# Performance work log

Hardware: AMD Instinct MI355X
Metric: run time of the kernel (lower is better)

Reference implementation:

```python
import jax, jax.numpy as jnp
import numpy as np

B = 512; S = 6; Q = 2            # meta-batch, n_way*k_shot, n_way*q_query
DIM = 64; IMG = 28; N_WAY = 2
HEADS = 4; HD = DIM // HEADS     # retrieval heads / head dim
EPS = 1e-5


def _pool_mat(inp, out):
    # exact torch AdaptiveAvgPool2d windowing as a matrix [out, inp]
    P = np.zeros((out, inp), np.float32)
    for i in range(out):
        s = (i * inp) // out
        e = -((-(i + 1) * inp) // out)
        P[i, s:e] = 1.0 / (e - s)
    return jnp.asarray(P)

P28 = _pool_mat(IMG, 8)  # 28 -> 8; subsequent 8 -> 8 pools are identity


def _gelu(x):
    return jax.nn.gelu(x, approximate=False)


def _conv(x, w, b):
    y = jax.lax.conv_general_dilated(x, w, (1, 1), ((1, 1), (1, 1)),
                                     dimension_numbers=('NCHW', 'OIHW', 'NCHW'))
    return y + b[None, :, None, None]


def _bn(x, p):
    # p rows: gamma, beta, running_mean, running_var (eval-mode BatchNorm2d)
    g, bt, m, v = p[0], p[1], p[2], p[3]
    sc = g / jnp.sqrt(v + EPS)
    return (x - m[None, :, None, None]) * sc[None, :, None, None] + bt[None, :, None, None]


def _img_in(x, c1w, c1b, bn1, c2w, c2b, bn2, c3w, c3b, bn3, c4w, c4b, bn4, lin_w):
    h = _bn(_conv(x, c1w, c1b), bn1)
    h = jnp.einsum('oi,ncij,pj->ncop', P28, h, P28)   # adaptive avg pool 28x28 -> 8x8
    h = _gelu(h)                                       # dropout is identity in eval
    h = _gelu(_bn(_conv(h, c2w, c2b), bn2))
    h = _gelu(_bn(_conv(h, c3w, c3b), bn3))
    h = _gelu(_bn(_conv(h, c4w, c4b), bn4))            # -> [N,1,8,8]
    h = h.reshape(h.shape[0], -1)                      # [N,64]
    return h @ lin_w.T                                 # Linear(64 -> DIM, no bias)


def _net(x, w1, w2):
    # x: [B,K,D]; w1,w2: [B,D,D] batched fast weights
    h = jnp.einsum('bed,bkd->bke', w1, x)
    ah = _gelu(h)
    y = jnp.einsum('bed,bkd->bke', w2, ah)
    return y, h


def _get_lor(x, w1, w2, r_q, r_k, r_v, r_o, ln_w, ln_b):
    b, k, _ = x.shape
    q, _ = _net(x, w1, w2)
    qh = jnp.einsum('nhd,bkd->bknh', r_q, q)
    sc = jnp.einsum('bknh,rnh->bknr', qh, r_k) / (HD ** 0.5)
    p = jax.nn.softmax(sc, axis=-1)
    lor = jnp.einsum('bknr,rnh->bknh', p, r_v).reshape(b, k, DIM)
    lor = jnp.einsum('de,bkd->bke', r_o, lor)
    z = lor + x
    mu = z.mean(-1, keepdims=True)
    var = ((z - mu) ** 2).mean(-1, keepdims=True)
    return (z - mu) / jnp.sqrt(var + EPS) * ln_w + ln_b


def _forward(query_w, sxs, qxs, inner_lr, c1w, c1b, bn1, c2w, c2b, bn2, c3w, c3b, bn3,
             c4w, c4b, bn4, lin_w, emb, w1, w2, tags, r_q, r_k, r_v, r_o, ln_w, ln_b,
             sys, qys):
    b = query_w.shape[0]
    s = sxs.shape[1]
    q = qxs.shape[1]
    feats = lambda im: _img_in(im.reshape(-1, 1, IMG, IMG), c1w, c1b, bn1, c2w, c2b,
                               bn2, c3w, c3b, bn3, c4w, c4b, bn4, lin_w)
    sx = feats(sxs).reshape(b, s, DIM)
    qx = feats(qxs).reshape(b, q, DIM)
    qe = tags[4]
    w1b = jnp.broadcast_to(w1, (b, DIM, DIM))
    w2b = jnp.broadcast_to(w2, (b, DIM, DIM))
    bound = sx + emb[sys]                                          # [B,S,D]
    # all 4 tag variants for all S shots in one vectorized get_lor call
    inp = (bound[:, :, None, :] + tags[:4][None, None]).reshape(b, s * 4, DIM)
    lors = _get_lor(inp, w1b, w2b, r_q, r_k, r_v, r_o, ln_w, ln_b).reshape(b, s, 4, DIM)
    l1s, r1s, l2s, r2s = lors[:, :, 0], lors[:, :, 1], lors[:, :, 2], lors[:, :, 3]
    qw1 = w1[None] + jnp.einsum('bsl,bsr->blr', l1s, r1s)
    qw2 = w2[None] + jnp.einsum('bsl,bsr->blr', l2s, r2s)
    preds, _ = _net(qx + qe, qw1, qw2)                             # [B,Q,D]
    logits = jnp.einsum('ld,bqd->bql', emb, preds).reshape(-1, N_WAY)
    labels = qys.reshape(-1)
    ls = jax.nn.log_softmax(logits)
    task_loss = -jnp.take_along_axis(ls, labels[:, None], axis=1).mean()
    n_correct = (jnp.argmax(logits, axis=1) == labels).sum()
    return task_loss, n_correct, b * q


def setup_inputs() -> dict:
    key = jax.random.key(0)
    ks = jax.random.split(key, 24)
    rn = lambda i, sh, sc=1.0: sc * jax.random.normal(ks[i], sh, jnp.float32)
    def bnp(i, c):
        k0, k1, k2 = jax.random.split(ks[i], 3)
        return jnp.stack([1.0 + 0.1 * jax.random.normal(k0, (c,)),
                          0.1 * jax.random.normal(k1, (c,)),
                          0.1 * jax.random.normal(k2, (c,)),
                          0.5 + jax.random.uniform(jax.random.fold_in(ks[i], 3), (c,))])
    return {
        'query_w': rn(0, (B, DIM)),
        'sxs': rn(1, (B, S, IMG * IMG)),
        'qxs': rn(2, (B, Q, IMG * IMG)),
        'inner_lr': jnp.float32(0.1),
        'c1w': rn(3, (32, 1, 3, 3), 0.3), 'c1b': rn(4, (32,), 0.1), 'bn1': bnp(5, 32),
        'c2w': rn(6, (32, 32, 3, 3), 0.06), 'c2b': rn(7, (32,), 0.1), 'bn2': bnp(8, 32),
        'c3w': rn(9, (32, 32, 3, 3), 0.06), 'c3b': rn(10, (32,), 0.1), 'bn3': bnp(11, 32),
        'c4w': rn(12, (1, 32, 3, 3), 0.06), 'c4b': rn(13, (1,), 0.1), 'bn4': bnp(14, 1),
        'lin_w': rn(15, (DIM, 64), 0.125),
        'emb': rn(16, (N_WAY, DIM), 0.125),
        'w1': rn(17, (DIM, DIM), 0.125),
        'w2': rn(18, (DIM, DIM), 0.125),
        'tags': rn(19, (8, DIM), 0.125),
        'r_q': rn(20, (HEADS, HD, DIM), 0.125),
        'r_k': rn(21, (16, HEADS, HD), 0.25),
        'r_v': rn(22, (16, HEADS, HD), 0.25),
        'r_o': rn(23, (DIM, DIM), 0.125),
        'ln_w': 0.001 * jnp.ones((DIM,), jnp.float32),
        'ln_b': jnp.zeros((DIM,), jnp.float32),
        'sys': jax.random.randint(jax.random.fold_in(key, 100), (B, S), 0, N_WAY),
        'qys': jax.random.randint(jax.random.fold_in(key, 101), (B, Q), 0, N_WAY),
    }


def reference(query_w, sxs, qxs, inner_lr, c1w, c1b, bn1, c2w, c2b, bn2, c3w, c3b, bn3,
              c4w, c4b, bn4, lin_w, emb, w1, w2, tags, r_q, r_k, r_v, r_o, ln_w, ln_b,
              sys, qys):
    task_loss, n_correct, n_q = _forward(query_w, sxs, qxs, inner_lr, c1w, c1b, bn1,
                                         c2w, c2b, bn2, c3w, c3b, bn3, c4w, c4b, bn4,
                                         lin_w, emb, w1, w2, tags, r_q, r_k, r_v, r_o,
                                         ln_w, ln_b, sys, qys)
    return (task_loss, task_loss, jnp.float32(0.0), n_correct, n_q)
```

## Files before the change

### kernel.cpp

```cpp
#include <hip/hip_runtime.h>
#include <math.h>

constexpr int NSUP = 3072;
constexpr float EPSF = 1e-5f;

constexpr int WS_W1B  = 0;
constexpr int WS_B1   = 1024;
constexpr int WS_W2B  = 1056;
constexpr int WS_W3B  = 5664;
constexpr int WS_W4B  = 10272;
constexpr int WS_B4   = 10416;
constexpr int WS_B2   = 10420;
constexpr int WS_B3   = 10452;
constexpr int WS_HW1  = 10484;
constexpr int WS_HW2  = 12788;
constexpr int WS_HRQ  = 15092;
constexpr int WS_HROT = 17396;
constexpr int WS_PART = 19700;
constexpr int WS_FEATS= 20724;

using short8 = __attribute__((ext_vector_type(8))) short;
using f32x4  = __attribute__((ext_vector_type(4))) float;

__device__ __forceinline__ float gelu_f(float x) {
    float z  = fabsf(x) * 0.70710678118654752440f;
    float t  = __builtin_amdgcn_rcpf(__builtin_fmaf(0.3275911f, z, 1.0f));
    float p  = t * __builtin_fmaf(t,
                 __builtin_fmaf(t,
                   __builtin_fmaf(t,
                     __builtin_fmaf(t, 1.061405429f, -1.453152027f),
                     1.421413741f),
                   -0.284496736f),
                 0.254829592f);
    float e  = __expf(-z * z);
    float er = __builtin_fmaf(-p, e, 1.0f);
    float s  = copysignf(er, x);
    return 0.5f * x * (1.0f + s);
}
__device__ __forceinline__ unsigned short f2bf(float f) {
    unsigned u = __float_as_uint(f);
    return (unsigned short)((u + 0x7FFFu + ((u >> 16) & 1u)) >> 16);
}
__device__ __forceinline__ float bflo(unsigned u) { return __uint_as_float(u << 16); }
__device__ __forceinline__ float bfhi(unsigned u) { return __uint_as_float(u & 0xffff0000u); }

__global__ void __launch_bounds__(256) precompute_kernel(
    const float* __restrict__ c1w, const float* __restrict__ c1b, const float* __restrict__ bn1,
    const float* __restrict__ c2w, const float* __restrict__ c2b, const float* __restrict__ bn2,
    const float* __restrict__ c3w, const float* __restrict__ c3b, const float* __restrict__ bn3,
    const float* __restrict__ c4w, const float* __restrict__ c4b, const float* __restrict__ bn4,
    const float* __restrict__ w1, const float* __restrict__ w2,
    const float* __restrict__ rq, const float* __restrict__ ro,
    float* __restrict__ ws)
{
    const int gid = blockIdx.x * 256 + threadIdx.x;
    const int gsz = gridDim.x * 256;

    unsigned short* w1b = (unsigned short*)(ws + WS_W1B);
    for (int v = gid; v < 2048; v += gsz) {
        int kt = v >> 10, rem = v & 1023, oc = rem >> 5, kk = rem & 31;
        int tap = kt * 32 + kk;
        unsigned short o = 0;
        if (tap < 36) {
            int tt = tap / 6, s = tap - tt * 6;
            float sum = 0.f;
            for (int di = 0; di < 3; ++di) {
                int a = tt - di; if (a < 0 || a > 3) continue;
                for (int dj = 0; dj < 3; ++dj) {
                    int bb = s - dj; if (bb < 0 || bb > 3) continue;
                    sum += c1w[oc * 9 + di * 3 + dj];
                }
            }
            float sc1 = bn1[oc] * rsqrtf(bn1[96 + oc] + EPSF);
            o = f2bf(sum * sc1 * (1.0f / 16.0f));
        }
        w1b[v] = o;
    }
    for (int c = gid; c < 32; c += gsz) {
        float sc1 = bn1[c] * rsqrtf(bn1[96 + c] + EPSF);
        ws[WS_B1 + c] = (c1b[c] - bn1[64 + c]) * sc1 + bn1[32 + c];
        float sc2 = bn2[c] * rsqrtf(bn2[96 + c] + EPSF);
        ws[WS_B2 + c] = (c2b[c] - bn2[64 + c]) * sc2 + bn2[32 + c];
        float sc3 = bn3[c] * rsqrtf(bn3[96 + c] + EPSF);
        ws[WS_B3 + c] = (c3b[c] - bn3[64 + c]) * sc3 + bn3[32 + c];
    }
    unsigned short* w2b = (unsigned short*)(ws + WS_W2B);
    unsigned short* w3b = (unsigned short*)(ws + WS_W3B);
    for (int v = gid; v < 9216; v += gsz) {
        int tap = v >> 10, oc = (v >> 5) & 31, ic = v & 31;
        float sc2 = bn2[oc] * rsqrtf(bn2[96 + oc] + EPSF);
        float sc3 = bn3[oc] * rsqrtf(bn3[96 + oc] + EPSF);
        w2b[v] = f2bf(c2w[oc * 288 + ic * 9 + tap] * sc2);
        w3b[v] = f2bf(c3w[oc * 288 + ic * 9 + tap] * sc3);
    }
    {
        unsigned short* w4b = (unsigned short*)(ws + WS_W4B);
        float sc4 = bn4[0] * rsqrtf(bn4[3] + EPSF);
        for (int v = gid; v < 288; v += gsz) {
            int tap = v >> 5, ic = v & 31;
            w4b[v] = f2bf(c4w[ic * 9 + tap] * sc4);
        }
        if (gid == 0) ws[WS_B4] = (c4b[0] - bn4[2]) * sc4 + bn4[1];
    }
    unsigned short* hw1 = (unsigned short*)(ws + WS_HW1);
    unsigned short* hw2 = (unsigned short*)(ws + WS_HW2);
    unsigned short* hrq = (unsigned short*)(ws + WS_HRQ);
    unsigned short* hro = (unsigned short*)(ws + WS_HROT);
    for (int v = gid; v < 4608; v += gsz) {
        int e = v / 72, d = v - e * 72;
        unsigned short a = 0, b = 0, c = 0, r = 0;
        if (d < 64) {
            a = f2bf(w1[e * 64 + d]);
            b = f2bf(w2[e * 64 + d]);
            c = f2bf(rq[e * 64 + d]);
            r = f2bf(ro[d * 64 + e]);
        }
        hw1[v] = a; hw2[v] = b; hrq[v] = c; hro[v] = r;
    }
}

__device__ __forceinline__ void conv32(unsigned short* __restrict__ A,
                                       const unsigned short* __restrict__ W,
                                       float bi0, float bi1, int col, int quad)
{
    f32x4 acc[4][2];
    #pragma unroll
    for (int mt = 0; mt < 4; ++mt) { acc[mt][0] = (f32x4){0,0,0,0}; acc[mt][1] = (f32x4){0,0,0,0}; }
    const unsigned short* abase[4];
    #pragma unroll
    for (int mt = 0; mt < 4; ++mt) {
        int px = mt * 16 + col;
        abase[mt] = A + ((px >> 3) * 10 + (px & 7)) * 32 + quad * 8;
    }
    #pragma unroll
    for (int dr = 0; dr < 3; ++dr)
        #pragma unroll
        for (int dc = 0; dc < 3; ++dc) {
            int tap = dr * 3 + dc;
            short8 b0 = *(const short8*)(W + (tap * 32 + col) * 32 + quad * 8);
            short8 b1 = *(const short8*)(W + (tap * 32 + 16 + col) * 32 + quad * 8);
            #pragma unroll
            for (int mt = 0; mt < 4; ++mt) {
                short8 a = *(const short8*)(abase[mt] + (dr * 10 + dc) * 32);
                acc[mt][0] = __builtin_amdgcn_mfma_f32_16x16x32_bf16(a, b0, acc[mt][0], 0, 0, 0);
                acc[mt][1] = __builtin_amdgcn_mfma_f32_16x16x32_bf16(a, b1, acc[mt][1], 0, 0, 0);
            }
        }
    #pragma unroll
    for (int mt = 0; mt < 4; ++mt)
        #pragma unroll
        for (int reg = 0; reg < 4; ++reg) {
            int px = mt * 16 + quad * 4 + reg;
            unsigned short* dst = A + (((px >> 3) + 1) * 10 + (px & 7) + 1) * 32;
            dst[col]      = f2bf(gelu_f(acc[mt][0][reg] + bi0));
            dst[col + 16] = f2bf(gelu_f(acc[mt][1][reg] + bi1));
        }
}

__global__ void __launch_bounds__(512, 4) feats_kernel(
    const float* __restrict__ sxs, const float* __restrict__ qxs,
    const float* __restrict__ lin_w, const float* __restrict__ ws,
    float* __restrict__ feats)
{
    __shared__ __align__(16) unsigned short sAct[8][3200];
    __shared__ __align__(16) unsigned short sWB[9216];
    __shared__ __align__(16) unsigned short sW4[288];
    __shared__ __align__(16) float sh4[8][64];

    const int t    = threadIdx.x;
    const int wv   = t >> 6;
    const int lane = t & 63;
    const int col  = lane & 15;
    const int quad = lane >> 4;
    const int n    = blockIdx.x * 8 + wv;

    unsigned short* A = sAct[wv];

    const uint4* w2v = (const uint4*)(ws + WS_W2B);
    uint4 pw0 = w2v[t];
    uint4 pw1 = w2v[t + 512];
    uint4 pw2 = {0, 0, 0, 0};
    if (t < 128) pw2 = w2v[t + 1024];

    {
        const float* img = (n < NSUP) ? (sxs + (size_t)n * 784) : (qxs + (size_t)(n - NSUP) * 784);
        const float4* sv = (const float4*)img;
        #pragma unroll
        for (int j = 0; j < 4; ++j) {
            int idx = j * 64 + lane;
            if (idx < 196) {
                float4 v = sv[idx];
                ushort4 o = { f2bf(v.x), f2bf(v.y), f2bf(v.z), f2bf(v.w) };
                *(ushort4*)(A + idx * 4) = o;
            }
        }
    }
    if (t < 256) ((uint4*)sWB)[t] = ((const uint4*)(ws + WS_W1B))[t];
    __syncthreads();

    {
        int ttj[8], ssj[8];
        #pragma unroll
        for (int j = 0; j < 8; ++j) {
            int k = quad * 8 + j;
            ttj[j] = k / 6; ssj[j] = k - ttj[j] * 6;
        }
        f32x4 acc[4][2];
        #pragma unroll
        for (int mt = 0; mt < 4; ++mt) { acc[mt][0] = (f32x4){0,0,0,0}; acc[mt][1] = (f32x4){0,0,0,0}; }

        short8 b00 = *(const short8*)(sWB + (0 * 32 + 0 * 16 + col) * 32 + quad * 8);
        short8 b01 = *(const short8*)(sWB + (0 * 32 + 1 * 16 + col) * 32 + quad * 8);
        short8 b10 = *(const short8*)(sWB + (1 * 32 + 0 * 16 + col) * 32 + quad * 8);
        short8 b11 = *(const short8*)(sWB + (1 * 32 + 1 * 16 + col) * 32 + quad * 8);

        #pragma unroll
        for (int mt = 0; mt < 4; ++mt) {
            int px = mt * 16 + col;
            int sr = (((px >> 3) * 7) >> 1) - 1;
            int sc = (((px & 7) * 7) >> 1) - 1;
            short8 a0;
            #pragma unroll
            for (int j = 0; j < 8; ++j) {
                int rr = sr + ttj[j], cc = sc + ssj[j];
                bool ok = ((unsigned)rr < 28u) && ((unsigned)cc < 28u);
                int off = ok ? (rr * 28 + cc) : 0;
                unsigned short hv = A[off];
                a0[j] = ok ? (short)hv : (short)0;
            }
            acc[mt][0] = __builtin_amdgcn_mfma_f32_16x16x32_bf16(a0, b00, acc[mt][0], 0, 0, 0);
            acc[mt][1] = __builtin_amdgcn_mfma_f32_16x16x32_bf16(a0, b01, acc[mt][1], 0, 0, 0);
            short8 a1 = {0,0,0,0,0,0,0,0};
            if (quad == 0) {
                #pragma unroll
                for (int j = 0; j < 4; ++j) {
                    int rr = sr + 5, cc = sc + 2 + j;
                    bool ok = ((unsigned)rr < 28u) && ((unsigned)cc < 28u);
                    int off = ok ? (rr * 28 + cc) : 0;
                    unsigned short hv = A[off];
                    a1[j] = ok ? (short)hv : (short)0;
                }
            }
            acc[mt][0] = __builtin_amdgcn_mfma_f32_16x16x32_bf16(a1, b10, acc[mt][0], 0, 0, 0);
            acc[mt][1] = __builtin_amdgcn_mfma_f32_16x16x32_bf16(a1, b11, acc[mt][1], 0, 0, 0);
        }

        {
            uint4 z4 = {0, 0, 0, 0};
            #pragma unroll
            for (int it = 0; it < 3; ++it) {
                int h = lane + it * 64;
                if (h < 144) {
                    int u4;
                    if (h < 40)      u4 = h;
                    else if (h < 80) u4 = 360 + (h - 40);
                    else {
                        int k = h - 80; int r = 1 + (k >> 3); int cj = k & 7;
                        u4 = r * 40 + ((cj >= 4) ? (32 + cj) : cj);
                    }
                    ((uint4*)A)[u4] = z4;
                }
            }
        }
        float bi0 = ws[WS_B1 + col], bi1 = ws[WS_B1 + 16 + col];
        #pragma unroll
        for (int mt = 0; mt < 4; ++mt)
            #pragma unroll
            for (int reg = 0; reg < 4; ++reg) {
                int px = mt * 16 + quad * 4 + reg;
                unsigned short* dst = A + (((px >> 3) + 1) * 10 + (px & 7) + 1) * 32;
                dst[col]      = f2bf(gelu_f(acc[mt][0][reg] + bi0));
                dst[col + 16] = f2bf(gelu_f(acc[mt][1][reg] + bi1));
            }
    }
    __syncthreads();

    {
        ((uint4*)sWB)[t]       = pw0;
        ((uint4*)sWB)[t + 512] = pw1;
        if (t < 128) ((uint4*)sWB)[t + 1024] = pw2;
        if (t < 36)  ((uint4*)sW4)[t] = ((const uint4*)(ws + WS_W4B))[t];
        const uint4* w3v = (const uint4*)(ws + WS_W3B);
        pw0 = w3v[t];
        pw1 = w3v[t + 512];
        if (t < 128) pw2 = w3v[t + 1024];
    }
    __syncthreads();

    conv32(A, sWB, ws[WS_B2 + col], ws[WS_B2 + 16 + col], col, quad);
    __syncthreads();
    {
        ((uint4*)sWB)[t]       = pw0;
        ((uint4*)sWB)[t + 512] = pw1;
        if (t < 128) ((uint4*)sWB)[t + 1024] = pw2;
    }
    __syncthreads();
    conv32(A, sWB, ws[WS_B3 + col], ws[WS_B3 + 16 + col], col, quad);

    {
        f32x4 acc4[4];
        #pragma unroll
        for (int mt = 0; mt < 4; ++mt) acc4[mt] = (f32x4){0,0,0,0};
        const unsigned short* abase[4];
        #pragma unroll
        for (int mt = 0; mt < 4; ++mt) {
            int px = mt * 16 + col;
            abase[mt] = A + ((px >> 3) * 10 + (px & 7)) * 32 + quad * 8;
        }
        #pragma unroll
        for (int dr = 0; dr < 3; ++dr)
            #pragma unroll
            for (int dc = 0; dc < 3; ++dc) {
                int tap = dr * 3 + dc;
                short8 b = *(const short8*)(sW4 + tap * 32 + quad * 8);
                #pragma unroll
                for (int mt = 0; mt < 4; ++mt) {
                    short8 a = *(const short8*)(abase[mt] + (dr * 10 + dc) * 32);
                    acc4[mt] = __builtin_amdgcn_mfma_f32_16x16x32_bf16(a, b, acc4[mt], 0, 0, 0);
                }
            }
        if (col < 4) {
            f32x4 v = acc4[0];
            if (col == 1) v = acc4[1];
            else if (col == 2) v = acc4[2];
            else if (col == 3) v = acc4[3];
            float b4 = ws[WS_B4];
            #pragma unroll
            for (int reg = 0; reg < 4; ++reg)
                sh4[wv][col * 16 + quad * 4 + reg] = gelu_f(v[reg] + b4);
        }
    }

    {
        const float4* lw = (const float4*)(lin_w + (size_t)lane * 64);
        const float4* hp = (const float4*)sh4[wv];
        float acc = 0.f;
        #pragma unroll
        for (int j = 0; j < 16; ++j) {
            float4 w = lw[j], h = hp[j];
            acc += w.x * h.x + w.y * h.y + w.z * h.z + w.w * h.w;
        }
        feats[n * 64 + lane] = acc;
    }
}

__device__ __forceinline__ void head_gemm(const unsigned short* __restrict__ Ab,
                                          const unsigned short* __restrict__ Bw,
                                          int col, int quad, int wvid, f32x4 res[2])
{
    #pragma unroll
    for (int u = 0; u < 2; ++u) {
        int tau = wvid + u * 4;
        int mt = tau & 1, nt = tau >> 1;
        f32x4 acc = {0, 0, 0, 0};
        #pragma unroll
        for (int kt = 0; kt < 2; ++kt) {
            short8 a = *(const short8*)(Ab + (mt * 16 + col) * 72 + kt * 32 + quad * 8);
            short8 b = *(const short8*)(Bw + (nt * 16 + col) * 72 + kt * 32 + quad * 8);
            acc = __builtin_amdgcn_mfma_f32_16x16x32_bf16(a, b, acc, 0, 0, 0);
        }
        res[u] = acc;
    }
}

__global__ void __launch_bounds__(256, 2) head_kernel(
    const float* __restrict__ emb, const float* __restrict__ tags,
    const float* __restrict__ rk, const float* __restrict__ rv,
    const float* __restrict__ lnw, const float* __restrict__ lnb,
    const int* __restrict__ sys, const int* __restrict__ qys,
    const float* __restrict__ ws, const float* __restrict__ feats,
    float* __restrict__ part)
{
    __shared__ __align__(16) unsigned short sW1B[4608], sW2B[4608], sRQB[4608], sROT[4608];
    __shared__ __align__(16) unsigned short bufA[2304], bufB[2304];
    __shared__ __align__(16) float sXf[1536];
    __shared__ __align__(16) float sRK[1024], sRV[1024];
    __shared__ __align__(16) float s_xq[128], s_ah[128], s_yp[128];
    __shared__ float s_t1[12], s_t2[12], s_mu[24], s_rs[24], s_lg[4];

    const int t    = threadIdx.x;
    const int b    = blockIdx.x;
    const int wvid = t >> 6;
    const int col  = t & 15;
    const int quad = (t >> 4) & 3;

    ((float4*)sRK)[t] = ((const float4*)rk)[t];
    ((float4*)sRV)[t] = ((const float4*)rv)[t];
    for (int i = t; i < 576; i += 256) {
        ((uint4*)sW1B)[i] = ((const uint4*)(ws + WS_HW1))[i];
        ((uint4*)sW2B)[i] = ((const uint4*)(ws + WS_HW2))[i];
        ((uint4*)sRQB)[i] = ((const uint4*)(ws + WS_HRQ))[i];
        ((uint4*)sROT)[i] = ((const uint4*)(ws + WS_HROT))[i];
    }
    if (t < 72) {
        uint4 z = {0, 0, 0, 0};
        ((uint4*)(bufA + 1728))[t] = z;
        ((uint4*)(bufB + 1728))[t] = z;
    }
    for (int idx = t; idx < 1536; idx += 256) {
        int k = idx >> 6, e = idx & 63;
        int s = k >> 2, tg = k & 3;
        int cls = sys[b * 6 + s];
        float v = feats[(b * 6 + s) * 64 + e] + emb[cls * 64 + e] + tags[tg * 64 + e];
        sXf[idx] = v;
        bufA[k * 72 + e] = f2bf(v);
    }
    __syncthreads();

    f32x4 r[2];
    head_gemm(bufA, sW1B, col, quad, wvid, r);
    #pragma unroll
    for (int u = 0; u < 2; ++u) {
        int tau = wvid + u * 4, mt = tau & 1, nt = tau >> 1;
        #pragma unroll
        for (int reg = 0; reg < 4; ++reg) {
            int row = mt * 16 + quad * 4 + reg;
            if (row < 24) bufB[row * 72 + nt * 16 + col] = f2bf(gelu_f(r[u][reg]));
        }
    }
    __syncthreads();
    head_gemm(bufB, sW2B, col, quad, wvid, r);
    #pragma unroll
    for (int u = 0; u < 2; ++u) {
        int tau = wvid + u * 4, mt = tau & 1, nt = tau >> 1;
        #pragma unroll
        for (int reg = 0; reg < 4; ++reg) {
            int row = mt * 16 + quad * 4 + reg;
            if (row < 24) bufA[row * 72 + nt * 16 + col] = f2bf(r[u][reg]);
        }
    }
    __syncthreads();
    head_gemm(bufA, sRQB, col, quad, wvid, r);
    #pragma unroll
    for (int u = 0; u < 2; ++u) {
        int tau = wvid + u * 4, mt = tau & 1, nt = tau >> 1;
        #pragma unroll
        for (int reg = 0; reg < 4; ++reg) {
            int row = mt * 16 + quad * 4 + reg;
            if (row < 24) bufB[row * 72 + nt * 16 + col] = f2bf(r[u][reg]);
        }
    }
    __syncthreads();

    if (t < 96) {
        int k = t >> 2, nn = t & 3;
        const unsigned short* qp = bufB + k * 72 + nn * 16;
        uint4 u0 = *(const uint4*)(qp);
        uint4 u1 = *(const uint4*)(qp + 8);
        float qv[16];
        qv[0]=bflo(u0.x); qv[1]=bfhi(u0.x); qv[2]=bflo(u0.y); qv[3]=bfhi(u0.y);
        qv[4]=bflo(u0.z); qv[5]=bfhi(u0.z); qv[6]=bflo(u0.w); qv[7]=bfhi(u0.w);
        qv[8]=bflo(u1.x); qv[9]=bfhi(u1.x); qv[10]=bflo(u1.y); qv[11]=bfhi(u1.y);
        qv[12]=bflo(u1.z); qv[13]=bfhi(u1.z); qv[14]=bflo(u1.w); qv[15]=bfhi(u1.w);
        float sc[16]; float mx = -1e30f;
        #pragma unroll
        for (int rr = 0; rr < 16; ++rr) {
            const float* kp = sRK + rr * 64 + nn * 16;
            float d = 0.f;
            #pragma unroll
            for (int h = 0; h < 16; ++h) d += qv[h] * kp[h];
            d *= 0.25f;
            sc[rr] = d; mx = fmaxf(mx, d);
        }
        float sum = 0.f;
        #pragma unroll
        for (int rr = 0; rr < 16; ++rr) { sc[rr] = __expf(sc[rr] - mx); sum += sc[rr]; }
        float inv = 1.0f / sum;
        float o[16];
        #pragma unroll
        for (int h = 0; h < 16; ++h) o[h] = 0.f;
        #pragma unroll
        for (int rr = 0; rr < 16; ++rr) {
            const float* vp = sRV + rr * 64 + nn * 16;
            float p = sc[rr];
            #pragma unroll
            for (int h = 0; h < 16; ++h) o[h] += p * vp[h];
        }
        unsigned short* op = bufA + k * 72 + nn * 16;
        #pragma unroll
        for (int h = 0; h < 16; ++h) op[h] = f2bf(o[h] * inv);
    }
    __syncthreads();

    head_gemm(bufA, sROT, col, quad, wvid, r);
    #pragma unroll
    for (int u = 0; u < 2; ++u) {
        int tau = wvid + u * 4, mt = tau & 1, nt = tau >> 1;
        #pragma unroll
        for (int reg = 0; reg < 4; ++reg) {
            int row = mt * 16 + quad * 4 + reg;
            if (row < 24) {
                int idx = row * 64 + nt * 16 + col;
                sXf[idx] = sXf[idx] + r[u][reg];
            }
        }
    }
    __syncthreads();

    if (t < 24) {
        const float4* zp = (const float4*)(sXf + t * 64);
        float sx_ = 0.f;
        #pragma unroll
        for (int j = 0; j < 16; ++j) {
            float4 v = zp[(j + t) & 15];
            sx_ += v.x + v.y + v.z + v.w;
        }
        float mu = sx_ * (1.0f / 64.0f);
        float vv = 0.f;
        #pragma unroll
        for (int j = 0; j < 16; ++j) {
            float4 v = zp[(j + t) & 15];
            float d0 = v.x - mu, d1 = v.y - mu, d2 = v.z - mu, d3 = v.w - mu;
            vv += d0*d0 + d1*d1 + d2*d2 + d3*d3;
        }
        s_mu[t] = mu;
        s_rs[t] = 1.0f / sqrtf(vv * (1.0f / 64.0f) + EPSF);
    }
    __syncthreads();
    for (int idx = t; idx < 1536; idx += 256) {
        int k = idx >> 6, e = idx & 63;
        float v = (sXf[idx] - s_mu[k]) * s_rs[k] * lnw[e] + lnb[e];
        bufB[k * 72 + e] = f2bf(v);
    }
    if (t < 128) {
        int q = t >> 6, e = t & 63;
        s_xq[t] = feats[(NSUP + b * 2 + q) * 64 + e] + tags[256 + e];
    }
    __syncthreads();

    if (t < 12) {
        int q = t / 6, s = t - q * 6;
        const uint4* rp = (const uint4*)(bufB + (s * 4 + 1) * 72);
        const float* xp = s_xq + q * 64;
        float d = 0.f;
        #pragma unroll
        for (int j = 0; j < 8; ++j) {
            uint4 u = rp[j];
            const float* x = xp + j * 8;
            d += bflo(u.x)*x[0] + bfhi(u.x)*x[1] + bflo(u.y)*x[2] + bfhi(u.y)*x[3]
               + bflo(u.z)*x[4] + bfhi(u.z)*x[5] + bflo(u.w)*x[6] + bfhi(u.w)*x[7];
        }
        s_t1[t] = d;
    }
    __syncthreads();
    if (t < 128) {
        int q = t >> 6, e = t & 63;
        const uint4* wp = (const uint4*)(sW1B + e * 72);
        const float* xp = s_xq + q * 64;
        float acc = 0.f;
        #pragma unroll
        for (int j = 0; j < 8; ++j) {
            uint4 u = wp[j];
            const float* x = xp + j * 8;
            acc += bflo(u.x)*x[0] + bfhi(u.x)*x[1] + bflo(u.y)*x[2] + bfhi(u.y)*x[3]
                 + bflo(u.z)*x[4] + bfhi(u.z)*x[5] + bflo(u.w)*x[6] + bfhi(u.w)*x[7];
        }
        #pragma unroll
        for (int s = 0; s < 6; ++s)
            acc += bflo((unsigned)bufB[(s * 4 + 0) * 72 + e]) * s_t1[q * 6 + s];
        s_ah[t] = gelu_f(acc);
    }
    __syncthreads();
    if (t < 12) {
        int q = t / 6, s = t - q * 6;
        const uint4* rp = (const uint4*)(bufB + (s * 4 + 3) * 72);
        const float* xp = s_ah + q * 64;
        float d = 0.f;
        #pragma unroll
        for (int j = 0; j < 8; ++j) {
            uint4 u = rp[j];
            const float* x = xp + j * 8;
            d += bflo(u.x)*x[0] + bfhi(u.x)*x[1] + bflo(u.y)*x[2] + bfhi(u.y)*x[3]
               + bflo(u.z)*x[4] + bfhi(u.z)*x[5] + bflo(u.w)*x[6] + bfhi(u.w)*x[7];
        }
        s_t2[t] = d;
    }
    __syncthreads();
    if (t < 128) {
        int q = t >> 6, e = t & 63;
        const uint4* wp = (const uint4*)(sW2B + e * 72);
        const float* xp = s_ah + q * 64;
        float acc = 0.f;
        #pragma unroll
        for (int j = 0; j < 8; ++j) {
            uint4 u = wp[j];
            const float* x = xp + j * 8;
            acc += bflo(u.x)*x[0] + bfhi(u.x)*x[1] + bflo(u.y)*x[2] + bfhi(u.y)*x[3]
                 + bflo(u.z)*x[4] + bfhi(u.z)*x[5] + bflo(u.w)*x[6] + bfhi(u.w)*x[7];
        }
        #pragma unroll
        for (int s = 0; s < 6; ++s)
            acc += bflo((unsigned)bufB[(s * 4 + 2) * 72 + e]) * s_t2[q * 6 + s];
        s_yp[t] = acc;
    }
    __syncthreads();
    if (t < 4) {
        int q = t >> 1, ll = t & 1;
        const float4* ep = (const float4*)(emb + ll * 64);
        const float4* yp = (const float4*)(s_yp + q * 64);
        float d = 0.f;
        #pragma unroll
        for (int j = 0; j < 16; ++j) {
            float4 a = ep[j], x = yp[j];
            d += a.x*x.x + a.y*x.y + a.z*x.z + a.w*x.w;
        }
        s_lg[t] = d;
    }
    __syncthreads();
    if (t == 0) {
        float lsum = 0.f, corr = 0.f;
        #pragma unroll
        for (int q = 0; q < 2; ++q) {
            float l0 = s_lg[q * 2], l1 = s_lg[q * 2 + 1];
            int lab = qys[b * 2 + q];
            float m = fmaxf(l0, l1);
            float lse = m + logf(expf(l0 - m) + expf(l1 - m));
            lsum += -((lab ? l1 : l0) - lse);
            int pred = (l1 > l0) ? 1 : 0;
            corr += (pred == lab) ? 1.0f : 0.0f;
        }
        part[b] = lsum;
        part[512 + b] = corr;
    }
}

__global__ void __launch_bounds__(256) finalize_kernel(const float* __restrict__ part,
                                                       float* __restrict__ out)
{
    __shared__ float sl[256], sc[256];
    const int t = threadIdx.x;
    sl[t] = part[t] + part[t + 256];
    sc[t] = part[512 + t] + part[768 + t];
    __syncthreads();
    for (int s = 128; s > 0; s >>= 1) {
        if (t < s) { sl[t] += sl[t + s]; sc[t] += sc[t + s]; }
        __syncthreads();
    }
    if (t == 0) {
        float loss = sl[0] * (1.0f / 1024.0f);
        out[0] = loss;
        out[1] = loss;
        out[2] = 0.0f;
        out[3] = sc[0];
        out[4] = 1024.0f;
    }
}

extern "C" void kernel_launch(void* const* d_in, const int* in_sizes, int n_in,
                              void* d_out, int out_size, void* d_ws, size_t ws_size,
                              hipStream_t stream)
{
    (void)in_sizes; (void)n_in; (void)out_size; (void)ws_size;
    const float* sxs  = (const float*)d_in[1];
    const float* qxs  = (const float*)d_in[2];
    const float* c1w  = (const float*)d_in[4];
    const float* c1b  = (const float*)d_in[5];
    const float* bn1  = (const float*)d_in[6];
    const float* c2w  = (const float*)d_in[7];
    const float* c2b  = (const float*)d_in[8];
    const float* bn2  = (const float*)d_in[9];
    const float* c3w  = (const float*)d_in[10];
    const float* c3b  = (const float*)d_in[11];
    const float* bn3  = (const float*)d_in[12];
    const float* c4w  = (const float*)d_in[13];
    const float* c4b  = (const float*)d_in[14];
    const float* bn4  = (const float*)d_in[15];
    const float* lin_w= (const float*)d_in[16];
    const float* emb  = (const float*)d_in[17];
    const float* w1   = (const float*)d_in[18];
    const float* w2   = (const float*)d_in[19];
    const float* tags = (const float*)d_in[20];
    const float* rq   = (const float*)d_in[21];
    const float* rk   = (const float*)d_in[22];
    const float* rv   = (const float*)d_in[23];
    const float* ro   = (const float*)d_in[24];
    const float* lnw  = (const float*)d_in[25];
    const float* lnb  = (const float*)d_in[26];
    const int*   sys  = (const int*)d_in[27];
    const int*   qys  = (const int*)d_in[28];

    float* ws  = (float*)d_ws;
    float* out = (float*)d_out;

    precompute_kernel<<<64, 256, 0, stream>>>(c1w, c1b, bn1, c2w, c2b, bn2,
                                              c3w, c3b, bn3, c4w, c4b, bn4,
                                              w1, w2, rq, ro, ws);
    feats_kernel<<<512, 512, 0, stream>>>(sxs, qxs, lin_w, ws, ws + WS_FEATS);
    head_kernel<<<512, 256, 0, stream>>>(emb, tags, rk, rv, lnw, lnb, sys, qys,
                                         ws, ws + WS_FEATS, ws + WS_PART);
    finalize_kernel<<<1, 256, 0, stream>>>(ws + WS_PART, out);
}
```

Before: 168.7 us.

## Restructure conv weights into MFMA fragment order and move retrieval attention onto MFMA

Conv weights are pre-permuted so each lane reads its MFMA B fragment straight from global memory (L2/L1). This removes the shared-memory weight staging and the block-wide barriers between conv layers. The activation buffer now uses a channel-chunk-major layout, and the feature kernel runs 4 waves per block instead of 8. In the head kernel, the retrieval softmax attention now uses bf16 MFMA with shuffle reductions instead of a per-thread scalar loop, and several small dot products and the layernorm statistics are spread across 8-lane shuffle reductions. The trade-off is repeated global/L1 loads of the weights per wave and extra bf16 rounding of the attention probabilities.

```diff
diff --git a/kernel.cpp b/kernel.cpp
--- a/kernel.cpp
+++ b/kernel.cpp
@@ -16,8 +16,10 @@
 constexpr int WS_HW2  = 12788;
 constexpr int WS_HRQ  = 15092;
 constexpr int WS_HROT = 17396;
-constexpr int WS_PART = 19700;
-constexpr int WS_FEATS= 20724;
+constexpr int WS_RKB  = 19700;
+constexpr int WS_RVT  = 20212;
+constexpr int WS_PART = 20724;
+constexpr int WS_FEATS= 21748;
 
 using short8 = __attribute__((ext_vector_type(8))) short;
 using f32x4  = __attribute__((ext_vector_type(4))) float;
@@ -51,6 +53,7 @@
     const float* __restrict__ c4w, const float* __restrict__ c4b, const float* __restrict__ bn4,
     const float* __restrict__ w1, const float* __restrict__ w2,
     const float* __restrict__ rq, const float* __restrict__ ro,
+    const float* __restrict__ rk, const float* __restrict__ rv,
     float* __restrict__ ws)
 {
     const int gid = blockIdx.x * 256 + threadIdx.x;
@@ -58,8 +61,9 @@
 
     unsigned short* w1b = (unsigned short*)(ws + WS_W1B);
     for (int v = gid; v < 2048; v += gsz) {
-        int kt = v >> 10, rem = v & 1023, oc = rem >> 5, kk = rem & 31;
-        int tap = kt * 32 + kk;
+        int c8 = v & 7, colx = (v >> 3) & 15, qd = (v >> 7) & 3, hh = (v >> 9) & 1, kt = v >> 10;
+        int tap = kt * 32 + qd * 8 + c8;
+        int oc = hh * 16 + colx;
         unsigned short o = 0;
         if (tap < 36) {
             int tt = tap / 6, s = tap - tt * 6;
@@ -87,7 +91,9 @@
     unsigned short* w2b = (unsigned short*)(ws + WS_W2B);
     unsigned short* w3b = (unsigned short*)(ws + WS_W3B);
     for (int v = gid; v < 9216; v += gsz) {
-        int tap = v >> 10, oc = (v >> 5) & 31, ic = v & 31;
+        int c8 = v & 7, colx = (v >> 3) & 15, qd = (v >> 7) & 3, hh = (v >> 9) & 1, tap = v >> 10;
+        int oc = hh * 16 + colx;
+        int ic = qd * 8 + c8;
         float sc2 = bn2[oc] * rsqrtf(bn2[96 + oc] + EPSF);
         float sc3 = bn3[oc] * rsqrtf(bn3[96 + oc] + EPSF);
         w2b[v] = f2bf(c2w[oc * 288 + ic * 9 + tap] * sc2);
@@ -117,70 +123,79 @@
         }
         hw1[v] = a; hw2[v] = b; hrq[v] = c; hro[v] = r;
     }
-}
-
-__device__ __forceinline__ void conv32(unsigned short* __restrict__ A,
-                                       const unsigned short* __restrict__ W,
-                                       float bi0, float bi1, int col, int quad)
-{
-    f32x4 acc[4][2];
-    #pragma unroll
-    for (int mt = 0; mt < 4; ++mt) { acc[mt][0] = (f32x4){0,0,0,0}; acc[mt][1] = (f32x4){0,0,0,0}; }
-    const unsigned short* abase[4];
+    unsigned short* rkb = (unsigned short*)(ws + WS_RKB);
+    unsigned short* rvt = (unsigned short*)(ws + WS_RVT);
+    for (int v = gid; v < 1024; v += gsz) {
+        int nn = v >> 8, x = (v >> 4) & 15, y = v & 15;
+        rkb[v] = f2bf(rk[x * 64 + nn * 16 + y] * 0.25f);
+        rvt[v] = f2bf(rv[y * 64 + nn * 16 + x]);
+    }
+}
+
+__device__ __forceinline__ void conv32g(const unsigned short* __restrict__ A,
+                                        const unsigned short* __restrict__ Wg,
+                                        int col, int quad, f32x4 (&acc)[4][2])
+{
+    int ab[4];
     #pragma unroll
     for (int mt = 0; mt < 4; ++mt) {
         int px = mt * 16 + col;
-        abase[mt] = A + ((px >> 3) * 10 + (px & 7)) * 32 + quad * 8;
+        ab[mt] = quad * 800 + ((px >> 3) * 10 + (px & 7)) * 8;
+        acc[mt][0] = (f32x4){0,0,0,0};
+        acc[mt][1] = (f32x4){0,0,0,0};
     }
     #pragma unroll
     for (int dr = 0; dr < 3; ++dr)
         #pragma unroll
         for (int dc = 0; dc < 3; ++dc) {
             int tap = dr * 3 + dc;
-            short8 b0 = *(const short8*)(W + (tap * 32 + col) * 32 + quad * 8);
-            short8 b1 = *(const short8*)(W + (tap * 32 + 16 + col) * 32 + quad * 8);
+            short8 b0 = *(const short8*)(Wg + (((tap * 2 + 0) * 4 + quad) * 16 + col) * 8);
+            short8 b1 = *(const short8*)(Wg + (((tap * 2 + 1) * 4 + quad) * 16 + col) * 8);
             #pragma unroll
             for (int mt = 0; mt < 4; ++mt) {
-                short8 a = *(const short8*)(abase[mt] + (dr * 10 + dc) * 32);
+                short8 a = *(const short8*)(A + ab[mt] + (dr * 10 + dc) * 8);
                 acc[mt][0] = __builtin_amdgcn_mfma_f32_16x16x32_bf16(a, b0, acc[mt][0], 0, 0, 0);
                 acc[mt][1] = __builtin_amdgcn_mfma_f32_16x16x32_bf16(a, b1, acc[mt][1], 0, 0, 0);
             }
         }
+}
+
+__device__ __forceinline__ void conv_store4(unsigned short* __restrict__ A,
+                                            const f32x4 (&acc)[4][2],
+                                            float bi0, float bi1, int col, int quad)
+{
     #pragma unroll
     for (int mt = 0; mt < 4; ++mt)
         #pragma unroll
         for (int reg = 0; reg < 4; ++reg) {
             int px = mt * 16 + quad * 4 + reg;
-            unsigned short* dst = A + (((px >> 3) + 1) * 10 + (px & 7) + 1) * 32;
-            dst[col]      = f2bf(gelu_f(acc[mt][0][reg] + bi0));
-            dst[col + 16] = f2bf(gelu_f(acc[mt][1][reg] + bi1));
-        }
-}
-
-__global__ void __launch_bounds__(512, 4) feats_kernel(
+            int P = ((px >> 3) + 1) * 10 + (px & 7) + 1;
+            A[(col >> 3) * 800 + P * 8 + (col & 7)]       = f2bf(gelu_f(acc[mt][0][reg] + bi0));
+            A[(2 + (col >> 3)) * 800 + P * 8 + (col & 7)] = f2bf(gelu_f(acc[mt][1][reg] + bi1));
+        }
+}
+
+__global__ void __launch_bounds__(256, 4) feats_kernel(
     const float* __restrict__ sxs, const float* __restrict__ qxs,
     const float* __restrict__ lin_w, const float* __restrict__ ws,
     float* __restrict__ feats)
 {
-    __shared__ __align__(16) unsigned short sAct[8][3200];
-    __shared__ __align__(16) unsigned short sWB[9216];
-    __shared__ __align__(16) unsigned short sW4[288];
-    __shared__ __align__(16) float sh4[8][64];
+    __shared__ __align__(16) unsigned short sAct[4][3200];
+    __shared__ __align__(16) float sh4[4][64];
 
     const int t    = threadIdx.x;
     const int wv   = t >> 6;
     const int lane = t & 63;
     const int col  = lane & 15;
     const int quad = lane >> 4;
-    const int n    = blockIdx.x * 8 + wv;
+    const int n    = blockIdx.x * 4 + wv;
 
     unsigned short* A = sAct[wv];
 
-    const uint4* w2v = (const uint4*)(ws + WS_W2B);
-    uint4 pw0 = w2v[t];
-    uint4 pw1 = w2v[t + 512];
-    uint4 pw2 = {0, 0, 0, 0};
-    if (t < 128) pw2 = w2v[t + 1024];
+    float bi1a = ws[WS_B1 + col], bi1b = ws[WS_B1 + 16 + col];
+    float bi2a = ws[WS_B2 + col], bi2b = ws[WS_B2 + 16 + col];
+    float bi3a = ws[WS_B3 + col], bi3b = ws[WS_B3 + 16 + col];
+    float b4   = ws[WS_B4];
 
     {
         const float* img = (n < NSUP) ? (sxs + (size_t)n * 784) : (qxs + (size_t)(n - NSUP) * 784);
@@ -195,27 +210,24 @@
             }
         }
     }
-    if (t < 256) ((uint4*)sWB)[t] = ((const uint4*)(ws + WS_W1B))[t];
-    __syncthreads();
-
-    {
+
+    f32x4 acc[4][2];
+    {
+        const unsigned short* w1g = (const unsigned short*)(ws + WS_W1B);
+        short8 b00 = *(const short8*)(w1g + ((0 * 4 + quad) * 16 + col) * 8);
+        short8 b01 = *(const short8*)(w1g + ((1 * 4 + quad) * 16 + col) * 8);
+        short8 b10 = *(const short8*)(w1g + ((2 * 4 + quad) * 16 + col) * 8);
+        short8 b11 = *(const short8*)(w1g + ((3 * 4 + quad) * 16 + col) * 8);
         int ttj[8], ssj[8];
         #pragma unroll
         for (int j = 0; j < 8; ++j) {
             int k = quad * 8 + j;
             ttj[j] = k / 6; ssj[j] = k - ttj[j] * 6;
         }
-        f32x4 acc[4][2];
-        #pragma unroll
-        for (int mt = 0; mt < 4; ++mt) { acc[mt][0] = (f32x4){0,0,0,0}; acc[mt][1] = (f32x4){0,0,0,0}; }
-
-        short8 b00 = *(const short8*)(sWB + (0 * 32 + 0 * 16 + col) * 32 + quad * 8);
-        short8 b01 = *(const short8*)(sWB + (0 * 32 + 1 * 16 + col) * 32 + quad * 8);
-        short8 b10 = *(const short8*)(sWB + (1 * 32 + 0 * 16 + col) * 32 + quad * 8);
-        short8 b11 = *(const short8*)(sWB + (1 * 32 + 1 * 16 + col) * 32 + quad * 8);
-
         #pragma unroll
         for (int mt = 0; mt < 4; ++mt) {
+            acc[mt][0] = (f32x4){0,0,0,0};
+            acc[mt][1] = (f32x4){0,0,0,0};
             int px = mt * 16 + col;
             int sr = (((px >> 3) * 7) >> 1) - 1;
             int sc = (((px & 7) * 7) >> 1) - 1;
@@ -244,78 +256,48 @@
             acc[mt][0] = __builtin_amdgcn_mfma_f32_16x16x32_bf16(a1, b10, acc[mt][0], 0, 0, 0);
             acc[mt][1] = __builtin_amdgcn_mfma_f32_16x16x32_bf16(a1, b11, acc[mt][1], 0, 0, 0);
         }
-
-        {
-            uint4 z4 = {0, 0, 0, 0};
-            #pragma unroll
-            for (int it = 0; it < 3; ++it) {
-                int h = lane + it * 64;
-                if (h < 144) {
-                    int u4;
-                    if (h < 40)      u4 = h;
-                    else if (h < 80) u4 = 360 + (h - 40);
-                    else {
-                        int k = h - 80; int r = 1 + (k >> 3); int cj = k & 7;
-                        u4 = r * 40 + ((cj >= 4) ? (32 + cj) : cj);
-                    }
-                    ((uint4*)A)[u4] = z4;
-                }
-            }
-        }
-        float bi0 = ws[WS_B1 + col], bi1 = ws[WS_B1 + 16 + col];
-        #pragma unroll
-        for (int mt = 0; mt < 4; ++mt)
-            #pragma unroll
-            for (int reg = 0; reg < 4; ++reg) {
-                int px = mt * 16 + quad * 4 + reg;
-                unsigned short* dst = A + (((px >> 3) + 1) * 10 + (px & 7) + 1) * 32;
-                dst[col]      = f2bf(gelu_f(acc[mt][0][reg] + bi0));
-                dst[col + 16] = f2bf(gelu_f(acc[mt][1][reg] + bi1));
-            }
-    }
-    __syncthreads();
-
-    {
-        ((uint4*)sWB)[t]       = pw0;
-        ((uint4*)sWB)[t + 512] = pw1;
-        if (t < 128) ((uint4*)sWB)[t + 1024] = pw2;
-        if (t < 36)  ((uint4*)sW4)[t] = ((const uint4*)(ws + WS_W4B))[t];
-        const uint4* w3v = (const uint4*)(ws + WS_W3B);
-        pw0 = w3v[t];
-        pw1 = w3v[t + 512];
-        if (t < 128) pw2 = w3v[t + 1024];
-    }
-    __syncthreads();
-
-    conv32(A, sWB, ws[WS_B2 + col], ws[WS_B2 + 16 + col], col, quad);
-    __syncthreads();
-    {
-        ((uint4*)sWB)[t]       = pw0;
-        ((uint4*)sWB)[t + 512] = pw1;
-        if (t < 128) ((uint4*)sWB)[t + 1024] = pw2;
-    }
-    __syncthreads();
-    conv32(A, sWB, ws[WS_B3 + col], ws[WS_B3 + 16 + col], col, quad);
+    }
+    {
+        uint4 z4 = {0, 0, 0, 0};
+        #pragma unroll
+        for (int it = 0; it < 3; ++it) {
+            int h = lane + it * 64;
+            if (h < 144) {
+                int pi = h >> 2, ch = h & 3;
+                int P;
+                if (pi < 10)      P = pi;
+                else if (pi < 20) P = 90 + (pi - 10);
+                else { int k = pi - 20; int r = 1 + (k >> 1); P = r * 10 + (k & 1) * 9; }
+                ((uint4*)A)[ch * 100 + P] = z4;
+            }
+        }
+    }
+    conv_store4(A, acc, bi1a, bi1b, col, quad);
+
+    conv32g(A, (const unsigned short*)(ws + WS_W2B), col, quad, acc);
+    conv_store4(A, acc, bi2a, bi2b, col, quad);
+    conv32g(A, (const unsigned short*)(ws + WS_W3B), col, quad, acc);
+    conv_store4(A, acc, bi3a, bi3b, col, quad);
 
     {
         f32x4 acc4[4];
-        #pragma unroll
-        for (int mt = 0; mt < 4; ++mt) acc4[mt] = (f32x4){0,0,0,0};
-        const unsigned short* abase[4];
+        int ab[4];
         #pragma unroll
         for (int mt = 0; mt < 4; ++mt) {
             int px = mt * 16 + col;
-            abase[mt] = A + ((px >> 3) * 10 + (px & 7)) * 32 + quad * 8;
-        }
+            ab[mt] = quad * 800 + ((px >> 3) * 10 + (px & 7)) * 8;
+            acc4[mt] = (f32x4){0,0,0,0};
+        }
+        const unsigned short* w4g = (const unsigned short*)(ws + WS_W4B);
         #pragma unroll
         for (int dr = 0; dr < 3; ++dr)
             #pragma unroll
             for (int dc = 0; dc < 3; ++dc) {
                 int tap = dr * 3 + dc;
-                short8 b = *(const short8*)(sW4 + tap * 32 + quad * 8);
+                short8 b = *(const short8*)(w4g + tap * 32 + quad * 8);
                 #pragma unroll
                 for (int mt = 0; mt < 4; ++mt) {
-                    short8 a = *(const short8*)(abase[mt] + (dr * 10 + dc) * 32);
+                    short8 a = *(const short8*)(A + ab[mt] + (dr * 10 + dc) * 8);
                     acc4[mt] = __builtin_amdgcn_mfma_f32_16x16x32_bf16(a, b, acc4[mt], 0, 0, 0);
                 }
             }
@@ -324,7 +306,6 @@
             if (col == 1) v = acc4[1];
             else if (col == 2) v = acc4[2];
             else if (col == 3) v = acc4[3];
-            float b4 = ws[WS_B4];
             #pragma unroll
             for (int reg = 0; reg < 4; ++reg)
                 sh4[wv][col * 16 + quad * 4 + reg] = gelu_f(v[reg] + b4);
@@ -334,13 +315,13 @@
     {
         const float4* lw = (const float4*)(lin_w + (size_t)lane * 64);
         const float4* hp = (const float4*)sh4[wv];
-        float acc = 0.f;
+        float acc2 = 0.f;
         #pragma unroll
         for (int j = 0; j < 16; ++j) {
             float4 w = lw[j], h = hp[j];
-            acc += w.x * h.x + w.y * h.y + w.z * h.z + w.w * h.w;
-        }
-        feats[n * 64 + lane] = acc;
+            acc2 += w.x * h.x + w.y * h.y + w.z * h.z + w.w * h.w;
+        }
+        feats[n * 64 + lane] = acc2;
     }
 }
 
@@ -365,7 +346,6 @@
 
 __global__ void __launch_bounds__(256, 2) head_kernel(
     const float* __restrict__ emb, const float* __restrict__ tags,
-    const float* __restrict__ rk, const float* __restrict__ rv,
     const float* __restrict__ lnw, const float* __restrict__ lnb,
     const int* __restrict__ sys, const int* __restrict__ qys,
     const float* __restrict__ ws, const float* __restrict__ feats,
@@ -373,8 +353,8 @@
 {
     __shared__ __align__(16) unsigned short sW1B[4608], sW2B[4608], sRQB[4608], sROT[4608];
     __shared__ __align__(16) unsigned short bufA[2304], bufB[2304];
+    __shared__ __align__(16) unsigned short sP[2048];
     __shared__ __align__(16) float sXf[1536];
-    __shared__ __align__(16) float sRK[1024], sRV[1024];
     __shared__ __align__(16) float s_xq[128], s_ah[128], s_yp[128];
     __shared__ float s_t1[12], s_t2[12], s_mu[24], s_rs[24], s_lg[4];
 
@@ -384,18 +364,20 @@
     const int col  = t & 15;
     const int quad = (t >> 4) & 3;
 
-    ((float4*)sRK)[t] = ((const float4*)rk)[t];
-    ((float4*)sRV)[t] = ((const float4*)rv)[t];
     for (int i = t; i < 576; i += 256) {
         ((uint4*)sW1B)[i] = ((const uint4*)(ws + WS_HW1))[i];
         ((uint4*)sW2B)[i] = ((const uint4*)(ws + WS_HW2))[i];
         ((uint4*)sRQB)[i] = ((const uint4*)(ws + WS_HRQ))[i];
         ((uint4*)sROT)[i] = ((const uint4*)(ws + WS_HROT))[i];
     }
-    if (t < 72) {
+    {
         uint4 z = {0, 0, 0, 0};
-        ((uint4*)(bufA + 1728))[t] = z;
-        ((uint4*)(bufB + 1728))[t] = z;
+        if (t < 72) {
+            ((uint4*)(bufA + 1728))[t] = z;
+            ((uint4*)(bufB + 1728))[t] = z;
+        }
+        if (t < 64)
+            ((uint4*)(sP + 1536))[t] = z;
     }
     for (int idx = t; idx < 1536; idx += 256) {
         int k = idx >> 6, e = idx & 63;
@@ -442,43 +424,49 @@
     }
     __syncthreads();
 
-    if (t < 96) {
-        int k = t >> 2, nn = t & 3;
-        const unsigned short* qp = bufB + k * 72 + nn * 16;
-        uint4 u0 = *(const uint4*)(qp);
-        uint4 u1 = *(const uint4*)(qp + 8);
-        float qv[16];
-        qv[0]=bflo(u0.x); qv[1]=bfhi(u0.x); qv[2]=bflo(u0.y); qv[3]=bfhi(u0.y);
-        qv[4]=bflo(u0.z); qv[5]=bfhi(u0.z); qv[6]=bflo(u0.w); qv[7]=bfhi(u0.w);
-        qv[8]=bflo(u1.x); qv[9]=bfhi(u1.x); qv[10]=bflo(u1.y); qv[11]=bfhi(u1.y);
-        qv[12]=bflo(u1.z); qv[13]=bfhi(u1.z); qv[14]=bflo(u1.w); qv[15]=bfhi(u1.w);
-        float sc[16]; float mx = -1e30f;
-        #pragma unroll
-        for (int rr = 0; rr < 16; ++rr) {
-            const float* kp = sRK + rr * 64 + nn * 16;
-            float d = 0.f;
-            #pragma unroll
-            for (int h = 0; h < 16; ++h) d += qv[h] * kp[h];
-            d *= 0.25f;
-            sc[rr] = d; mx = fmaxf(mx, d);
-        }
-        float sum = 0.f;
-        #pragma unroll
-        for (int rr = 0; rr < 16; ++rr) { sc[rr] = __expf(sc[rr] - mx); sum += sc[rr]; }
-        float inv = 1.0f / sum;
-        float o[16];
-        #pragma unroll
-        for (int h = 0; h < 16; ++h) o[h] = 0.f;
-        #pragma unroll
-        for (int rr = 0; rr < 16; ++rr) {
-            const float* vp = sRV + rr * 64 + nn * 16;
-            float p = sc[rr];
-            #pragma unroll
-            for (int h = 0; h < 16; ++h) o[h] += p * vp[h];
-        }
-        unsigned short* op = bufA + k * 72 + nn * 16;
-        #pragma unroll
-        for (int h = 0; h < 16; ++h) op[h] = f2bf(o[h] * inv);
+    {
+        const int nh = wvid;
+        const unsigned short* rkB = (const unsigned short*)(ws + WS_RKB) + nh * 256;
+        const unsigned short* rvT = (const unsigned short*)(ws + WS_RVT) + nh * 256;
+        const short8 zz = {0,0,0,0,0,0,0,0};
+        const bool lo = (quad < 2);
+        short8 bK = lo ? *(const short8*)(rkB + col * 16 + quad * 8) : zz;
+        short8 a0 = lo ? *(const short8*)(bufB + col * 72 + nh * 16 + quad * 8) : zz;
+        short8 a1 = lo ? *(const short8*)(bufB + (16 + col) * 72 + nh * 16 + quad * 8) : zz;
+        f32x4 s0 = __builtin_amdgcn_mfma_f32_16x16x32_bf16(a0, bK, (f32x4){0,0,0,0}, 0, 0, 0);
+        f32x4 s1 = __builtin_amdgcn_mfma_f32_16x16x32_bf16(a1, bK, (f32x4){0,0,0,0}, 0, 0, 0);
+        #pragma unroll
+        for (int reg = 0; reg < 4; ++reg) {
+            float v = s0[reg];
+            float m = v;
+            m = fmaxf(m, __shfl_xor(m, 1)); m = fmaxf(m, __shfl_xor(m, 2));
+            m = fmaxf(m, __shfl_xor(m, 4)); m = fmaxf(m, __shfl_xor(m, 8));
+            float p = __expf(v - m);
+            float su = p;
+            su += __shfl_xor(su, 1); su += __shfl_xor(su, 2);
+            su += __shfl_xor(su, 4); su += __shfl_xor(su, 8);
+            sP[(quad * 4 + reg) * 64 + nh * 16 + col] = f2bf(p / su);
+            v = s1[reg];
+            m = v;
+            m = fmaxf(m, __shfl_xor(m, 1)); m = fmaxf(m, __shfl_xor(m, 2));
+            m = fmaxf(m, __shfl_xor(m, 4)); m = fmaxf(m, __shfl_xor(m, 8));
+            p = __expf(v - m);
+            su = p;
+            su += __shfl_xor(su, 1); su += __shfl_xor(su, 2);
+            su += __shfl_xor(su, 4); su += __shfl_xor(su, 8);
+            if (quad < 2) sP[(16 + quad * 4 + reg) * 64 + nh * 16 + col] = f2bf(p / su);
+        }
+        short8 bV  = lo ? *(const short8*)(rvT + col * 16 + quad * 8) : zz;
+        short8 pa0 = lo ? *(const short8*)(sP + col * 64 + nh * 16 + quad * 8) : zz;
+        short8 pa1 = lo ? *(const short8*)(sP + (16 + col) * 64 + nh * 16 + quad * 8) : zz;
+        f32x4 o0 = __builtin_amdgcn_mfma_f32_16x16x32_bf16(pa0, bV, (f32x4){0,0,0,0}, 0, 0, 0);
+        f32x4 o1 = __builtin_amdgcn_mfma_f32_16x16x32_bf16(pa1, bV, (f32x4){0,0,0,0}, 0, 0, 0);
+        #pragma unroll
+        for (int reg = 0; reg < 4; ++reg) {
+            bufA[(quad * 4 + reg) * 72 + nh * 16 + col] = f2bf(o0[reg]);
+            int tok = 16 + quad * 4 + reg;
+            if (tok < 24) bufA[tok * 72 + nh * 16 + col] = f2bf(o1[reg]);
+        }
     }
     __syncthreads();
 
@@ -497,24 +485,21 @@
     }
     __syncthreads();
 
-    if (t < 24) {
-        const float4* zp = (const float4*)(sXf + t * 64);
-        float sx_ = 0.f;
-        #pragma unroll
-        for (int j = 0; j < 16; ++j) {
-            float4 v = zp[(j + t) & 15];
-            sx_ += v.x + v.y + v.z + v.w;
-        }
+    if (t < 192) {
+        int k = t >> 3, j = t & 7;
+        const float4* zp = (const float4*)(sXf + k * 64 + j * 8);
+        float4 v0 = zp[0], v1 = zp[1];
+        float sx_ = v0.x + v0.y + v0.z + v0.w + v1.x + v1.y + v1.z + v1.w;
+        sx_ += __shfl_xor(sx_, 1); sx_ += __shfl_xor(sx_, 2); sx_ += __shfl_xor(sx_, 4);
         float mu = sx_ * (1.0f / 64.0f);
-        float vv = 0.f;
-        #pragma unroll
-        for (int j = 0; j < 16; ++j) {
-            float4 v = zp[(j + t) & 15];
-            float d0 = v.x - mu, d1 = v.y - mu, d2 = v.z - mu, d3 = v.w - mu;
-            vv += d0*d0 + d1*d1 + d2*d2 + d3*d3;
-        }
-        s_mu[t] = mu;
-        s_rs[t] = 1.0f / sqrtf(vv * (1.0f / 64.0f) + EPSF);
+        float d0 = v0.x - mu, d1 = v0.y - mu, d2 = v0.z - mu, d3 = v0.w - mu;
+        float d4 = v1.x - mu, d5 = v1.y - mu, d6 = v1.z - mu, d7 = v1.w - mu;
+        float vv = d0*d0 + d1*d1 + d2*d2 + d3*d3 + d4*d4 + d5*d5 + d6*d6 + d7*d7;
+        vv += __shfl_xor(vv, 1); vv += __shfl_xor(vv, 2); vv += __shfl_xor(vv, 4);
+        if (j == 0) {
+            s_mu[k] = mu;
+            s_rs[k] = 1.0f / sqrtf(vv * (1.0f / 64.0f) + EPSF);
+        }
     }
     __syncthreads();
     for (int idx = t; idx < 1536; idx += 256) {
@@ -528,19 +513,15 @@
     }
     __syncthreads();
 
-    if (t < 12) {
-        int q = t / 6, s = t - q * 6;
-        const uint4* rp = (const uint4*)(bufB + (s * 4 + 1) * 72);
-        const float* xp = s_xq + q * 64;
-        float d = 0.f;
-        #pragma unroll
-        for (int j = 0; j < 8; ++j) {
-            uint4 u = rp[j];
-            const float* x = xp + j * 8;
-            d += bflo(u.x)*x[0] + bfhi(u.x)*x[1] + bflo(u.y)*x[2] + bfhi(u.y)*x[3]
-               + bflo(u.z)*x[4] + bfhi(u.z)*x[5] + bflo(u.w)*x[6] + bfhi(u.w)*x[7];
-        }
-        s_t1[t] = d;
+    if (t < 96) {
+        int idx = t >> 3, j = t & 7;
+        int q = idx / 6, s = idx - q * 6;
+        uint4 u = ((const uint4*)(bufB + (s * 4 + 1) * 72))[j];
+        const float* x = s_xq + q * 64 + j * 8;
+        float d = bflo(u.x)*x[0] + bfhi(u.x)*x[1] + bflo(u.y)*x[2] + bfhi(u.y)*x[3]
+                + bflo(u.z)*x[4] + bfhi(u.z)*x[5] + bflo(u.w)*x[6] + bfhi(u.w)*x[7];
+        d += __shfl_xor(d, 1); d += __shfl_xor(d, 2); d += __shfl_xor(d, 4);
+        if (j == 0) s_t1[idx] = d;
     }
     __syncthreads();
     if (t < 128) {
@@ -561,19 +542,15 @@
         s_ah[t] = gelu_f(acc);
     }
     __syncthreads();
-    if (t < 12) {
-        int q = t / 6, s = t - q * 6;
-        const uint4* rp = (const uint4*)(bufB + (s * 4 + 3) * 72);
-        const float* xp = s_ah + q * 64;
-        float d = 0.f;
-        #pragma unroll
-        for (int j = 0; j < 8; ++j) {
-            uint4 u = rp[j];
-            const float* x = xp + j * 8;
-            d += bflo(u.x)*x[0] + bfhi(u.x)*x[1] + bflo(u.y)*x[2] + bfhi(u.y)*x[3]
-               + bflo(u.z)*x[4] + bfhi(u.z)*x[5] + bflo(u.w)*x[6] + bfhi(u.w)*x[7];
-        }
-        s_t2[t] = d;
+    if (t < 96) {
+        int idx = t >> 3, j = t & 7;
+        int q = idx / 6, s = idx - q * 6;
+        uint4 u = ((const uint4*)(bufB + (s * 4 + 3) * 72))[j];
+        const float* x = s_ah + q * 64 + j * 8;
+        float d = bflo(u.x)*x[0] + bfhi(u.x)*x[1] + bflo(u.y)*x[2] + bfhi(u.y)*x[3]
+                + bflo(u.z)*x[4] + bfhi(u.z)*x[5] + bflo(u.w)*x[6] + bfhi(u.w)*x[7];
+        d += __shfl_xor(d, 1); d += __shfl_xor(d, 2); d += __shfl_xor(d, 4);
+        if (j == 0) s_t2[idx] = d;
     }
     __syncthreads();
     if (t < 128) {
@@ -594,17 +571,14 @@
         s_yp[t] = acc;
     }
     __syncthreads();
-    if (t < 4) {
-        int q = t >> 1, ll = t & 1;
-        const float4* ep = (const float4*)(emb + ll * 64);
-        const float4* yp = (const float4*)(s_yp + q * 64);
-        float d = 0.f;
-        #pragma unroll
-        for (int j = 0; j < 16; ++j) {
-            float4 a = ep[j], x = yp[j];
-            d += a.x*x.x + a.y*x.y + a.z*x.z + a.w*x.w;
-        }
-        s_lg[t] = d;
+    if (t < 32) {
+        int q = t >> 4, ll = (t >> 3) & 1, j = t & 7;
+        const float* ep = emb + ll * 64 + j * 8;
+        const float* yp = s_yp + q * 64 + j * 8;
+        float d = ep[0]*yp[0] + ep[1]*yp[1] + ep[2]*yp[2] + ep[3]*yp[3]
+                + ep[4]*yp[4] + ep[5]*yp[5] + ep[6]*yp[6] + ep[7]*yp[7];
+        d += __shfl_xor(d, 1); d += __shfl_xor(d, 2); d += __shfl_xor(d, 4);
+        if (j == 0) s_lg[q * 2 + ll] = d;
     }
     __syncthreads();
     if (t == 0) {
@@ -684,9 +658,9 @@
 
     precompute_kernel<<<64, 256, 0, stream>>>(c1w, c1b, bn1, c2w, c2b, bn2,
                                               c3w, c3b, bn3, c4w, c4b, bn4,
-                                              w1, w2, rq, ro, ws);
-    feats_kernel<<<512, 512, 0, stream>>>(sxs, qxs, lin_w, ws, ws + WS_FEATS);
-    head_kernel<<<512, 256, 0, stream>>>(emb, tags, rk, rv, lnw, lnb, sys, qys,
+                                              w1, w2, rq, ro, rk, rv, ws);
+    feats_kernel<<<1024, 256, 0, stream>>>(sxs, qxs, lin_w, ws, ws + WS_FEATS);
+    head_kernel<<<512, 256, 0, stream>>>(emb, tags, lnw, lnb, sys, qys,
                                          ws, ws + WS_FEATS, ws + WS_PART);
     finalize_kernel<<<1, 256, 0, stream>>>(ws + WS_PART, out);
 }
```

After: 167.8 us, median of 3. Within noise of the previous version (-0.6%).
